# Optimization experiments

Measured on AMD Instinct MI355X. Metric: run time of the kernel, lower is better.

## Reference

```python
import jax, jax.numpy as jnp
import numpy as np
import math

NEG = -1e9


def maximum_path(logp, mask):
    # logp, mask: [B, Tx, Ty]; Viterbi-style monotonic alignment search (VITS MAS)
    B, Tx, Ty = logp.shape
    lp = jnp.where(mask > 0, logp, NEG)
    # forward DP: value[x, y] = lp[x, y] + max(value[x, y-1], value[x-1, y-1])
    v0 = jnp.where(jnp.arange(Tx)[None, :] == 0, lp[:, :, 0], NEG)  # [B, Tx]

    def fwd(v, lp_y):
        v_diag = jnp.pad(v[:, :-1], ((0, 0), (1, 0)), constant_values=NEG)
        take_diag = v_diag > v  # strict >, matches cython 'value[x,y-1] < value[x-1,y-1]'
        return lp_y + jnp.maximum(v, v_diag), take_diag

    lp_rest = jnp.moveaxis(lp[:, :, 1:], 2, 0)  # [Ty-1, B, Tx]
    _, dirs = jax.lax.scan(fwd, v0, lp_rest)
    dirs = jnp.concatenate([jnp.zeros((1, B, Tx), bool), dirs], axis=0)  # [Ty, B, Tx]

    t_x = mask[:, :, 0].sum(axis=1).astype(jnp.int32)  # valid text length per batch
    t_y = mask[:, 0, :].sum(axis=1).astype(jnp.int32)  # valid spec length per batch

    def back(idx, inp):
        dir_y, y = inp  # dir_y [B, Tx], y scalar
        active = (y < t_y)  # [B]
        row = jax.nn.one_hot(idx, Tx, dtype=logp.dtype) * active[:, None].astype(logp.dtype)
        d = jnp.take_along_axis(dir_y, idx[:, None], axis=1)[:, 0]
        idx = jnp.where(active, idx - d.astype(jnp.int32), idx)
        return idx, row

    ys = jnp.arange(Ty - 1, -1, -1)
    _, rows = jax.lax.scan(back, t_x - 1, (dirs[::-1], ys))
    path = jnp.moveaxis(rows[::-1], 0, 2)  # [B, Tx, Ty]
    return path


def _make_masks(x_lengths, y_lengths, Tx, Ty):
    x_len = jnp.clip(x_lengths, 2, Tx)
    y_len = jnp.clip(y_lengths, 2, Ty)
    y_len = jnp.maximum(y_len, x_len)  # MAS needs T_y >= T_x per sample
    x_mask = (jnp.arange(Tx)[None, :] < x_len[:, None]).astype(jnp.float32)  # [B, Tx]
    y_mask = (jnp.arange(Ty)[None, :] < y_len[:, None]).astype(jnp.float32)  # [B, Ty]
    return x_mask, y_mask


def setup_inputs() -> dict:
    key = jax.random.key(0)
    B, C, Tx, Ty = 32, 192, 512, 2048
    k1, k2, k3, k4, k5 = jax.random.split(key, 5)
    z_p = jax.random.normal(k1, (B, C, Ty), dtype=jnp.float32)
    m_p = jax.random.normal(k2, (B, C, Tx), dtype=jnp.float32)
    logs_p = jax.random.normal(k3, (B, C, Tx), dtype=jnp.float32) * 0.3
    x_lengths = jax.random.randint(k4, (B,), Tx // 2, Tx + 1, dtype=jnp.int32)
    y_lengths = jax.random.randint(k5, (B,), Ty // 2, Ty + 1, dtype=jnp.int32)
    return {"z_p": z_p, "m_p": m_p, "logs_p": logs_p, "x_lengths": x_lengths, "y_lengths": y_lengths}


def reference(z_p, m_p, logs_p, x_lengths, y_lengths):
    B, C, Ty = z_p.shape
    Tx = m_p.shape[2]
    x_mask, y_mask = _make_masks(x_lengths, y_lengths, Tx, Ty)
    attn_mask = x_mask[:, :, None] * y_mask[:, None, :]  # [B, Tx, Ty]

    # log N(z_p ; m_p, exp(logs_p)) scored for every (text, spec) pair
    o_scale = jnp.exp(-2.0 * logs_p)  # [B, C, Tx]
    logp1 = jnp.sum(-0.5 * math.log(2.0 * math.pi) - logs_p, axis=1)[:, :, None]  # [B, Tx, 1]
    logp2 = jnp.einsum('bct,bcs->bts', o_scale, -0.5 * z_p ** 2)  # [B, Tx, Ty]
    logp3 = jnp.einsum('bct,bcs->bts', m_p * o_scale, z_p)
    logp4 = jnp.sum(-0.5 * m_p ** 2 * o_scale, axis=1)[:, :, None]
    logp = logp2 + logp3 + logp1 + logp4

    attn = maximum_path(logp, attn_mask)  # [B, Tx, Ty], hard 0/1 alignment
    attn_durations = attn.sum(axis=2)[:, None, :]  # [B, 1, Tx]

    # expand text stats to spec frames: torch.einsum('klmn,kjm->kjn', attn[:,None], m_p)
    m_p_dur = jnp.einsum('bts,bct->bcs', attn, m_p)      # [B, C, Ty]
    logs_p_dur = jnp.einsum('bts,bct->bcs', attn, logs_p)
    return attn_durations, attn[:, None], m_p_dur, logs_p_dur
```

## Files before the change

kernel.cpp:

```cpp
#include <hip/hip_runtime.h>

#define NEGV -1e9f
#define BB 32
#define CC 192
#define TXD 512
#define TYD 2048

#define E_DUR   0
#define E_ATTN  16384
#define E_MP    33570816
#define E_LS    46153728
#define E_TOTAL 58736640

#define OFF_DIRS  6291456

#define WS_PATH 0ull
#define WS_YST  131072ull
#define WS_TXTY 196864ull
#define WS_NEED 262144ull

typedef _Float16 f16x8 __attribute__((ext_vector_type(8)));
typedef float f32x4 __attribute__((ext_vector_type(4)));

__device__ __forceinline__ void glds16(const void* g, void* l) {
    __builtin_amdgcn_global_load_lds((const __attribute__((address_space(1))) unsigned*)g,
                                     (__attribute__((address_space(3))) unsigned*)l, 16, 0, 0);
}
__device__ __forceinline__ unsigned packh(_Float16 a, _Float16 b) {
    union { _Float16 h[2]; unsigned u; } x; x.h[0] = a; x.h[1] = b; return x.u;
}

__global__ __launch_bounds__(256) void k_prepB(const float* __restrict__ logs_p,
                                               const float* __restrict__ m_p,
                                               const int* __restrict__ xl,
                                               const int* __restrict__ yl,
                                               _Float16* __restrict__ Bpl,
                                               float* __restrict__ l14,
                                               unsigned* __restrict__ txty) {
    __shared__ float lst[CC][33];
    __shared__ float mst[CC][33];
    __shared__ float p14[8][32];
    int b = blockIdx.y, t0 = blockIdx.x * 32, tid = threadIdx.x;
    const float* lsb = logs_p + (size_t)b * CC * TXD + t0;
    const float* mb  = m_p    + (size_t)b * CC * TXD + t0;
#pragma unroll
    for (int i = 0; i < 24; ++i) {
        int u = i * 256 + tid, c = u >> 5, t = u & 31;
        lst[c][t] = lsb[(size_t)c * TXD + t];
        mst[c][t] = mb [(size_t)c * TXD + t];
    }
    __syncthreads();
    { int q = tid >> 5, t = tid & 31; float s = 0.f;
      for (int c = q * 24; c < q * 24 + 24; ++c) {
          float ls = lst[c][t], m = mst[c][t];
          float o = expf(-2.f * ls);
          s += -0.918938533204672741780329736406f - ls - 0.5f * m * m * o;
      }
      p14[q][t] = s; }
    __syncthreads();
    if (tid < 32) {
        float s = 0.f;
#pragma unroll
        for (int q = 0; q < 8; ++q) s += p14[q][tid];
        l14[b * TXD + t0 + tid] = s;
    }
    _Float16* Bb = Bpl + (size_t)b * (4 * TXD * CC);
    unsigned* B0 = (unsigned*)(Bb);
    unsigned* B1 = (unsigned*)(Bb + (size_t)1 * TXD * CC);
    unsigned* B2 = (unsigned*)(Bb + (size_t)2 * TXD * CC);
    unsigned* B3 = (unsigned*)(Bb + (size_t)3 * TXD * CC);
#pragma unroll
    for (int i = 0; i < 12; ++i) {
        int u = i * 256 + tid, t = u / 96, cp = u - t * 96, c = cp * 2;
        float ls0 = lst[c][t], ls1 = lst[c + 1][t];
        float m0 = mst[c][t], m1 = mst[c + 1][t];
        float o0 = expf(-2.f * ls0), o1 = expf(-2.f * ls1);
        float w0 = m0 * o0, w1 = m1 * o1;
        _Float16 oh0 = (_Float16)o0, oh1 = (_Float16)o1;
        _Float16 ol0 = (_Float16)(o0 - (float)oh0), ol1 = (_Float16)(o1 - (float)oh1);
        _Float16 wh0 = (_Float16)w0, wh1 = (_Float16)w1;
        _Float16 wl0 = (_Float16)(w0 - (float)wh0), wl1 = (_Float16)(w1 - (float)wh1);
        int ui = ((t0 + t) * CC + c) >> 1;
        B0[ui] = packh(oh0, oh1);
        B1[ui] = packh(ol0, ol1);
        B2[ui] = packh(wh0, wh1);
        B3[ui] = packh(wl0, wl1);
    }
    if (blockIdx.x == 0 && blockIdx.y == 0 && tid < BB) {
        int txv = min(max(xl[tid], 2), TXD);
        int tyv = min(max(yl[tid], 2), TYD);
        tyv = max(tyv, txv);
        txty[tid] = (unsigned)txv;
        txty[BB + tid] = (unsigned)tyv;
    }
}

__global__ __launch_bounds__(256) void k_prepZ(const float* __restrict__ z_p,
                                               _Float16* __restrict__ Zpl, int sBase) {
    __shared__ float zt[CC][65];
    int b = blockIdx.y, s0 = blockIdx.x * 64, tid = threadIdx.x;
    const float* zb = z_p + (size_t)b * CC * TYD + sBase + s0;
#pragma unroll
    for (int i = 0; i < 48; ++i) {
        int u = i * 256 + tid, c = u >> 6, s = u & 63;
        zt[c][s] = zb[(size_t)c * TYD + s];
    }
    __syncthreads();
    _Float16* Zb = Zpl + (size_t)b * (4 * 1024 * CC);
    unsigned* Z0 = (unsigned*)(Zb);
    unsigned* Z1 = (unsigned*)(Zb + (size_t)1 * 1024 * CC);
    unsigned* Z2 = (unsigned*)(Zb + (size_t)2 * 1024 * CC);
    unsigned* Z3 = (unsigned*)(Zb + (size_t)3 * 1024 * CC);
#pragma unroll
    for (int i = 0; i < 24; ++i) {
        int u = i * 256 + tid, s = u / 96, cp = u - s * 96, c = cp * 2;
        float z0 = zt[c][s], z1 = zt[c + 1][s];
        float P0 = -0.5f * z0 * z0, P1 = -0.5f * z1 * z1;
        _Float16 ph0 = (_Float16)P0, ph1 = (_Float16)P1;
        _Float16 pl0 = (_Float16)(P0 - (float)ph0), pl1 = (_Float16)(P1 - (float)ph1);
        _Float16 zh0 = (_Float16)z0, zh1 = (_Float16)z1;
        _Float16 zl0 = (_Float16)(z0 - (float)zh0), zl1 = (_Float16)(z1 - (float)zh1);
        int ui = ((s0 + s) * CC + c) >> 1;
        Z0[ui] = packh(ph0, ph1);
        Z1[ui] = packh(pl0, pl1);
        Z2[ui] = packh(zh0, zh1);
        Z3[ui] = packh(zl0, zl1);
    }
}

__global__ __launch_bounds__(256, 2) void k_mm(const _Float16* __restrict__ Zpl,
                                               const _Float16* __restrict__ Bpl,
                                               const float* __restrict__ l14,
                                               const unsigned* __restrict__ txty,
                                               float* __restrict__ L, int sBase) {
    __shared__ __align__(16) char As[32768];
    __shared__ __align__(16) char Bs[16384];
    int bid = blockIdx.x;
    int xcd = bid & 7, idx = bid >> 3;
    int b = xcd + 8 * (idx >> 4);
    int tile = idx & 15;
    int s0 = (tile >> 2) * 256, t0 = (tile & 3) * 128;
    int txb = (int)txty[b], tyb = (int)txty[BB + b];
    int sg0 = sBase + s0;
    if (sg0 >= tyb) return;
    int tid = threadIdx.x, l = tid & 63, w = tid >> 6;
    float* Lt = L + ((size_t)b * TYD + sg0) * TXD + t0;
    if (t0 >= txb) {
#pragma unroll
        for (int i = 0; i < 32; ++i) {
            int u = i * 256 + tid, r = u >> 5, c4 = (u & 31) * 4;
            *(float4*)(Lt + (size_t)r * TXD + c4) = make_float4(NEGV, NEGV, NEGV, NEGV);
        }
        return;
    }
    f32x4 acc[4][8];
#pragma unroll
    for (int i = 0; i < 4; ++i)
#pragma unroll
        for (int j = 0; j < 8; ++j) acc[i][j] = (f32x4){0.f, 0.f, 0.f, 0.f};

    const char* Zb = (const char*)(Zpl + (size_t)b * (4 * 1024 * CC));
    const char* Bb = (const char*)(Bpl + (size_t)b * (4 * TXD * CC));
    int lrow = l >> 3;
    int gOff = lrow * 384 + (((l & 7) ^ lrow) * 16);
    int arow_off = (w * 64 + (l & 15)) * 128;
    int brow_off = (l & 15) * 128;
    int slot0 = (((l >> 4) + 0) ^ (l & 7)) * 16;
    int slot1 = (((l >> 4) + 4) ^ (l & 7)) * 16;

    for (int pass = 0; pass < 6; ++pass) {
        int ap = ((pass >= 3) ? 2 : 0) + ((pass == 2 || pass == 5) ? 1 : 0);
        int bp = ((pass >= 3) ? 2 : 0) + ((pass == 1 || pass == 4) ? 1 : 0);
        const char* Zp = Zb + ((size_t)ap * 1024 + s0) * 384;
        const char* Bp = Bb + ((size_t)bp * TXD + t0) * 384;
        for (int k0 = 0; k0 < 384; k0 += 128) {
            __syncthreads();
#pragma unroll
            for (int j = 0; j < 8; ++j) {
                int c = w * 8 + j;
                glds16(Zp + (size_t)c * (8 * 384) + gOff + k0, As + c * 1024);
            }
#pragma unroll
            for (int j = 0; j < 4; ++j) {
                int c = w * 4 + j;
                glds16(Bp + (size_t)c * (8 * 384) + gOff + k0, Bs + c * 1024);
            }
            __syncthreads();
#pragma unroll
            for (int ks = 0; ks < 2; ++ks) {
                int so = ks ? slot1 : slot0;
                f16x8 av[4], bv[8];
#pragma unroll
                for (int fm = 0; fm < 4; ++fm)
                    av[fm] = *(const f16x8*)(As + arow_off + fm * (16 * 128) + so);
#pragma unroll
                for (int fn = 0; fn < 8; ++fn)
                    bv[fn] = *(const f16x8*)(Bs + brow_off + fn * (16 * 128) + so);
#pragma unroll
                for (int fm = 0; fm < 4; ++fm)
#pragma unroll
                    for (int fn = 0; fn < 8; ++fn)
                        acc[fm][fn] = __builtin_amdgcn_mfma_f32_16x16x32_f16(
                            av[fm], bv[fn], acc[fm][fn], 0, 0, 0);
            }
        }
    }
    float l14v[8];
#pragma unroll
    for (int fn = 0; fn < 8; ++fn) l14v[fn] = l14[b * TXD + t0 + fn * 16 + (l & 15)];
    int sb = sg0 + w * 64 + (l >> 4) * 4;
    int tcol = t0 + (l & 15);
#pragma unroll
    for (int fm = 0; fm < 4; ++fm)
#pragma unroll
        for (int r = 0; r < 4; ++r) {
            int sg = sb + fm * 16 + r;
            bool sv = sg < tyb;
            float* Lrow = L + ((size_t)b * TYD + sg) * TXD;
#pragma unroll
            for (int fn = 0; fn < 8; ++fn) {
                int t = tcol + fn * 16;
                Lrow[t] = (sv && t < txb) ? (acc[fm][fn][r] + l14v[fn]) : NEGV;
            }
        }
}

__global__ __launch_bounds__(64) void k_dp(const float* __restrict__ L,
                                           const unsigned* __restrict__ txty,
                                           unsigned* __restrict__ dirsG,
                                           unsigned short* __restrict__ pathG,
                                           unsigned* __restrict__ ystartG,
                                           float* __restrict__ outDur) {
    __shared__ unsigned char dmaps[32 * 512];
    __shared__ unsigned short path[TYD];
    __shared__ unsigned cnt[513];
    __shared__ unsigned ebuf[32];
    int b = blockIdx.x, lane = threadIdx.x;
    int tx = (int)txty[b], ty = (int)txty[BB + b];
    const float* Lb = L + (size_t)b * (TYD * TXD);
    unsigned* dGw = dirsG + (size_t)b * (512 * 64);

    float4 aLo[8], aHi[8], bLo[8], bHi[8];
    float v[8];
    unsigned p[8];
    int G8 = (ty + 7) >> 3;

#define LOAD_GRP(LO, HI, GN) do {                                           \
        _Pragma("unroll")                                                   \
        for (int q_ = 0; q_ < 8; ++q_) {                                    \
            int r_ = 8 * (GN) + q_;                                         \
            r_ = (r_ < ty) ? r_ : (ty - 1);                                 \
            const float* rp_ = Lb + (size_t)r_ * TXD + lane * 8;            \
            LO[q_] = *(const float4*)(rp_);                                 \
            HI[q_] = *(const float4*)(rp_ + 4);                             \
        } } while (0)

#define DP_GRP(LO, HI, G_) do {                                             \
        unsigned w0_ = 0, w1_ = 0;                                          \
        _Pragma("unroll")                                                   \
        for (int q_ = 0; q_ < 8; ++q_) {                                    \
            int y_ = 8 * (G_) + q_;                                         \
            if ((G_) == 0 && q_ == 0) {                                     \
                float lp_[8] = {LO[0].x, LO[0].y, LO[0].z, LO[0].w,         \
                                HI[0].x, HI[0].y, HI[0].z, HI[0].w};        \
                _Pragma("unroll")                                           \
                for (int i = 0; i < 8; ++i) {                               \
                    int x_ = lane * 8 + i;                                  \
                    v[i] = (x_ == 0) ? lp_[i] : NEGV;                       \
                    p[i] = (unsigned)x_;                                    \
                }                                                           \
            } else if (y_ < ty) {                                           \
                float cur_[8] = {LO[q_].x, LO[q_].y, LO[q_].z, LO[q_].w,    \
                                 HI[q_].x, HI[q_].y, HI[q_].z, HI[q_].w};   \
                float vp0_ = __int_as_float(__builtin_amdgcn_mov_dpp(       \
                    __float_as_int(v[7]), 0x138, 0xf, 0xf, true));          \
                unsigned pp0_ = (unsigned)__builtin_amdgcn_mov_dpp(         \
                    (int)p[7], 0x138, 0xf, 0xf, true);                      \
                if (lane == 0) vp0_ = NEGV;                                 \
                unsigned bits_ = 0;                                         \
                _Pragma("unroll")                                           \
                for (int i = 7; i >= 0; --i) {                              \
                    float vp_ = (i == 0) ? vp0_ : v[i - 1];                 \
                    unsigned pp_ = (i == 0) ? pp0_ : p[i - 1];              \
                    bool d_ = vp_ > v[i];                                   \
                    v[i] = cur_[i] + (d_ ? vp_ : v[i]);                     \
                    p[i] = d_ ? pp_ : p[i];                                 \
                    bits_ |= (d_ ? 1u : 0u) << i;                           \
                }                                                           \
                if (q_ < 4) w0_ |= bits_ << (8 * q_);                       \
                else        w1_ |= bits_ << (8 * (q_ - 4));                 \
                if (q_ == 0 && ((G_) & 7) == 0 && (G_) != 0) {              \
                    _Pragma("unroll")                                       \
                    for (int i = 0; i < 8; ++i) p[i] = (unsigned)(lane * 8 + i); \
                }                                                           \
                if (q_ == 7 && ((G_) & 7) == 7) {                           \
                    int c_ = y_ >> 6;                                       \
                    _Pragma("unroll")                                       \
                    for (int i = 0; i < 8; ++i)                             \
                        dmaps[c_ * 512 + lane * 8 + i] =                    \
                            (unsigned char)((unsigned)(lane * 8 + i) - p[i]); \
                }                                                           \
            }                                                               \
        }                                                                   \
        dGw[(2 * (G_)) * 64 + lane] = w0_;                                  \
        dGw[(2 * (G_) + 1) * 64 + lane] = w1_;                              \
        } while (0)

    LOAD_GRP(aLo, aHi, 0);
    LOAD_GRP(bLo, bHi, 1);
    for (int g = 0; g < G8; g += 2) {
        DP_GRP(aLo, aHi, g);
        LOAD_GRP(aLo, aHi, g + 2);
        if (g + 1 < G8) {
            DP_GRP(bLo, bHi, g + 1);
            LOAD_GRP(bLo, bHi, g + 3);
        }
    }
#undef LOAD_GRP
#undef DP_GRP
    __syncthreads();

    int c0 = (ty - 1) >> 6;
    if (lane == 0) {
        int pos = tx - 1;
        for (int y = ty - 1; y >= (c0 << 6); --y) {
            path[y] = (unsigned short)pos;
            unsigned wv = dGw[(y >> 2) * 64 + (pos >> 3)];
            pos -= (int)((wv >> (((y & 3) << 3) | (pos & 7))) & 1u);
        }
        for (int c = c0 - 1; c >= 0; --c) {
            ebuf[c] = (unsigned)pos;
            int P = pos - (int)dmaps[c * 512 + pos];
            unsigned wv = dGw[(c << 4) * 64 + (P >> 3)];
            pos = P - (int)((wv >> (P & 7)) & 1u);
        }
    }
    __syncthreads();
    if (lane < c0) {
        int c = lane;
        int pos = (int)ebuf[c];
        for (int y = (c << 6) + 63; y >= (c << 6); --y) {
            path[y] = (unsigned short)pos;
            unsigned wv = dGw[(y >> 2) * 64 + (pos >> 3)];
            pos -= (int)((wv >> (((y & 3) << 3) | (pos & 7))) & 1u);
        }
    }
    __syncthreads();

    for (int i = lane; i < 513; i += 64) cnt[i] = 0;
    __syncthreads();
    for (int y = lane; y < ty; y += 64) atomicAdd(&cnt[path[y]], 1u);
    __syncthreads();

    unsigned c8[8], lsum = 0;
#pragma unroll
    for (int i = 0; i < 8; ++i) {
        c8[i] = cnt[lane * 8 + i];
        lsum += c8[i];
    }
    unsigned incl = lsum;
    for (int d = 1; d < 64; d <<= 1) {
        unsigned t = (unsigned)__shfl_up((int)incl, d);
        if (lane >= d) incl += t;
    }
    unsigned run = incl - lsum;
#pragma unroll
    for (int i = 0; i < 8; ++i) {
        int x = lane * 8 + i;
        ystartG[b * 513 + x] = run;
        outDur[(size_t)b * TXD + x] = (float)c8[i];
        run += c8[i];
    }
    if (lane == 0) ystartG[b * 513 + 512] = (unsigned)ty;
    for (int y = lane; y < ty; y += 64) pathG[b * TYD + y] = path[y];
}

__global__ __launch_bounds__(64) void k_attn(const unsigned* __restrict__ ystartG,
                                             float* __restrict__ out) {
    int x = blockIdx.x, b = blockIdx.y, lane = threadIdx.x;
    unsigned s0 = ystartG[b * 513 + x];
    unsigned s1 = ystartG[b * 513 + x + 1];
    float* row = out + E_ATTN + ((size_t)(b * TXD + x)) * TYD + lane * 32;
#pragma unroll
    for (int k = 0; k < 8; ++k) {
        unsigned y0 = (unsigned)(lane * 32 + k * 4);
        float4 o;
        o.x = (y0 + 0 >= s0 && y0 + 0 < s1) ? 1.0f : 0.0f;
        o.y = (y0 + 1 >= s0 && y0 + 1 < s1) ? 1.0f : 0.0f;
        o.z = (y0 + 2 >= s0 && y0 + 2 < s1) ? 1.0f : 0.0f;
        o.w = (y0 + 3 >= s0 && y0 + 3 < s1) ? 1.0f : 0.0f;
        *(float4*)(row + k * 4) = o;
    }
}

__global__ __launch_bounds__(256) void k_gather(const float* __restrict__ m_p,
                                                const float* __restrict__ logs_p,
                                                const unsigned short* __restrict__ pathG,
                                                const unsigned* __restrict__ txty,
                                                float* __restrict__ out) {
    __shared__ unsigned short px[64];
    int yc = blockIdx.x, b = blockIdx.y;
    int y0 = yc * 64, tid = threadIdx.x;
    int lane = tid & 63, w = tid >> 6;
    int ty = (int)txty[BB + b];
    if (tid < 64) px[tid] = (y0 + tid < ty) ? pathG[b * TYD + y0 + tid] : 0;
    __syncthreads();
    bool act = (y0 + lane) < ty;
    int xx = (int)px[lane];
    for (int c = w; c < CC; c += 4) {
        float mv = act ? m_p[((size_t)b * CC + c) * TXD + xx] : 0.0f;
        float lv = act ? logs_p[((size_t)b * CC + c) * TXD + xx] : 0.0f;
        size_t oidx = ((size_t)(b * CC + c)) * TYD + y0 + lane;
        out[E_MP + oidx] = mv;
        out[E_LS + oidx] = lv;
    }
}

extern "C" void kernel_launch(void* const* d_in, const int* in_sizes, int n_in,
                              void* d_out, int out_size, void* d_ws, size_t ws_size,
                              hipStream_t stream) {
    if (out_size < E_TOTAL) return;
    if (ws_size < WS_NEED) return;
    const float* z_p    = (const float*)d_in[0];
    const float* m_p    = (const float*)d_in[1];
    const float* logs_p = (const float*)d_in[2];
    const int* xl       = (const int*)d_in[3];
    const int* yl       = (const int*)d_in[4];
    float* out = (float*)d_out;
    char* ws = (char*)d_ws;

    float* l14            = out + E_DUR;
    float* L              = out + E_ATTN;
    _Float16* Zpl         = (_Float16*)(out + E_MP);
    _Float16* Bpl         = (_Float16*)(out + E_LS);
    unsigned* dirsG       = (unsigned*)(out + E_LS + OFF_DIRS);
    unsigned short* pathG = (unsigned short*)(ws + WS_PATH);
    unsigned* ystartG     = (unsigned*)(ws + WS_YST);
    unsigned* txty        = (unsigned*)(ws + WS_TXTY);

    hipLaunchKernelGGL(k_prepB, dim3(16, BB), dim3(256), 0, stream,
                       logs_p, m_p, xl, yl, Bpl, l14, txty);
    hipLaunchKernelGGL(k_prepZ, dim3(16, BB), dim3(256), 0, stream, z_p, Zpl, 0);
    hipLaunchKernelGGL(k_mm, dim3(512), dim3(256), 0, stream, Zpl, Bpl, l14, txty, L, 0);
    hipLaunchKernelGGL(k_prepZ, dim3(16, BB), dim3(256), 0, stream, z_p, Zpl, 1024);
    hipLaunchKernelGGL(k_mm, dim3(512), dim3(256), 0, stream, Zpl, Bpl, l14, txty, L, 1024);
    hipLaunchKernelGGL(k_dp, dim3(BB), dim3(64), 0, stream, L, txty, dirsG, pathG, ystartG, out + E_DUR);
    hipLaunchKernelGGL(k_attn, dim3(TXD, BB), dim3(64), 0, stream, ystartG, out);
    hipLaunchKernelGGL(k_gather, dim3(TYD / 64, BB), dim3(256), 0, stream, m_p, logs_p, pathG, txty, out);
}
```

Measured before the change: 545.5 us.

## Add prefetch helper wavefront to DP kernel to warm cache ahead of scan

The DP kernel grows from one to two wavefronts. The second wave walks the L matrix one phase (16 groups of 8 rows) ahead of the compute wave, touching one float per 64-byte line to pull rows into cache. The two waves stay in step through a per-phase __syncthreads. The DP inner step also computes the max with fmaxf instead of a select. This aims to hide global-memory latency on the latency-bound serial scan, at the cost of barrier overhead and extra memory traffic.

Result: slower. 581.9 us (+6.7%).

```diff
diff --git a/kernel.cpp b/kernel.cpp
--- a/kernel.cpp
+++ b/kernel.cpp
@@ -225,25 +225,28 @@
         }
 }
 
-__global__ __launch_bounds__(64) void k_dp(const float* __restrict__ L,
-                                           const unsigned* __restrict__ txty,
-                                           unsigned* __restrict__ dirsG,
-                                           unsigned short* __restrict__ pathG,
-                                           unsigned* __restrict__ ystartG,
-                                           float* __restrict__ outDur) {
+__global__ __launch_bounds__(128) void k_dp(const float* __restrict__ L,
+                                            const unsigned* __restrict__ txty,
+                                            unsigned* __restrict__ dirsG,
+                                            unsigned short* __restrict__ pathG,
+                                            unsigned* __restrict__ ystartG,
+                                            float* __restrict__ outDur) {
     __shared__ unsigned char dmaps[32 * 512];
     __shared__ unsigned short path[TYD];
     __shared__ unsigned cnt[513];
     __shared__ unsigned ebuf[32];
-    int b = blockIdx.x, lane = threadIdx.x;
+    int b = blockIdx.x, tid = threadIdx.x;
+    int lane = tid & 63, wid = tid >> 6;
     int tx = (int)txty[b], ty = (int)txty[BB + b];
     const float* Lb = L + (size_t)b * (TYD * TXD);
     unsigned* dGw = dirsG + (size_t)b * (512 * 64);
-
-    float4 aLo[8], aHi[8], bLo[8], bHi[8];
-    float v[8];
-    unsigned p[8];
     int G8 = (ty + 7) >> 3;
+    int nPhase = (G8 + 15) >> 4;
+
+    if (wid == 0) {
+        float4 aLo[8], aHi[8], bLo[8], bHi[8];
+        float v[8];
+        unsigned p[8];
 
 #define LOAD_GRP(LO, HI, GN) do {                                           \
         _Pragma("unroll")                                                   \
@@ -282,8 +285,9 @@
                 for (int i = 7; i >= 0; --i) {                              \
                     float vp_ = (i == 0) ? vp0_ : v[i - 1];                 \
                     unsigned pp_ = (i == 0) ? pp0_ : p[i - 1];              \
-                    bool d_ = vp_ > v[i];                                   \
-                    v[i] = cur_[i] + (d_ ? vp_ : v[i]);                     \
+                    float vm_ = fmaxf(vp_, v[i]);     \
+                    bool d_ = vp_ > v[i];             \
+                    v[i] = cur_[i] + vm_;                                   \
                     p[i] = d_ ? pp_ : p[i];                                 \
                     bits_ |= (d_ ? 1u : 0u) << i;                           \
                 }                                                           \
@@ -306,22 +310,45 @@
         dGw[(2 * (G_) + 1) * 64 + lane] = w1_;                              \
         } while (0)
 
-    LOAD_GRP(aLo, aHi, 0);
-    LOAD_GRP(bLo, bHi, 1);
-    for (int g = 0; g < G8; g += 2) {
-        DP_GRP(aLo, aHi, g);
-        LOAD_GRP(aLo, aHi, g + 2);
-        if (g + 1 < G8) {
-            DP_GRP(bLo, bHi, g + 1);
-            LOAD_GRP(bLo, bHi, g + 3);
-        }
-    }
+        LOAD_GRP(aLo, aHi, 0);
+        LOAD_GRP(bLo, bHi, 1);
+        int g = 0;
+        for (int ph = 0; ph < nPhase; ++ph) {
+            __syncthreads();
+            int gEnd = (ph + 1) << 4; if (gEnd > G8) gEnd = G8;
+            for (; g < gEnd; g += 2) {
+                DP_GRP(aLo, aHi, g);
+                LOAD_GRP(aLo, aHi, g + 2);
+                if (g + 1 < G8) {
+                    DP_GRP(bLo, bHi, g + 1);
+                    LOAD_GRP(bLo, bHi, g + 3);
+                }
+            }
+        }
 #undef LOAD_GRP
 #undef DP_GRP
+    } else {
+        const char* Lc = (const char*)Lb;
+        float acc = 0.f;
+        for (int gp = 0; gp < 16 && gp < G8; ++gp) {
+            const float* fp = (const float*)(Lc + (size_t)gp * 16384 + (lane << 6));
+            acc += fp[0] + fp[1024] + fp[2048] + fp[3072];
+        }
+        for (int ph = 0; ph < nPhase; ++ph) {
+            __syncthreads();
+            int a = (ph + 1) << 4, bnd = (ph + 2) << 4;
+            if (bnd > G8) bnd = G8;
+            for (int gp = a; gp < bnd; ++gp) {
+                const float* fp = (const float*)(Lc + (size_t)gp * 16384 + (lane << 6));
+                acc += fp[0] + fp[1024] + fp[2048] + fp[3072];
+            }
+        }
+        asm volatile("" :: "v"(acc));
+    }
     __syncthreads();
 
     int c0 = (ty - 1) >> 6;
-    if (lane == 0) {
+    if (tid == 0) {
         int pos = tx - 1;
         for (int y = ty - 1; y >= (c0 << 6); --y) {
             path[y] = (unsigned short)pos;
@@ -336,8 +363,8 @@
         }
     }
     __syncthreads();
-    if (lane < c0) {
-        int c = lane;
+    if (tid < c0) {
+        int c = tid;
         int pos = (int)ebuf[c];
         for (int y = (c << 6) + 63; y >= (c << 6); --y) {
             path[y] = (unsigned short)pos;
@@ -347,32 +374,34 @@
     }
     __syncthreads();
 
-    for (int i = lane; i < 513; i += 64) cnt[i] = 0;
-    __syncthreads();
-    for (int y = lane; y < ty; y += 64) atomicAdd(&cnt[path[y]], 1u);
-    __syncthreads();
-
-    unsigned c8[8], lsum = 0;
-#pragma unroll
-    for (int i = 0; i < 8; ++i) {
-        c8[i] = cnt[lane * 8 + i];
-        lsum += c8[i];
-    }
-    unsigned incl = lsum;
-    for (int d = 1; d < 64; d <<= 1) {
-        unsigned t = (unsigned)__shfl_up((int)incl, d);
-        if (lane >= d) incl += t;
-    }
-    unsigned run = incl - lsum;
-#pragma unroll
-    for (int i = 0; i < 8; ++i) {
-        int x = lane * 8 + i;
-        ystartG[b * 513 + x] = run;
-        outDur[(size_t)b * TXD + x] = (float)c8[i];
-        run += c8[i];
-    }
-    if (lane == 0) ystartG[b * 513 + 512] = (unsigned)ty;
-    for (int y = lane; y < ty; y += 64) pathG[b * TYD + y] = path[y];
+    for (int i = tid; i < 513; i += 128) cnt[i] = 0;
+    __syncthreads();
+    for (int y = tid; y < ty; y += 128) atomicAdd(&cnt[path[y]], 1u);
+    __syncthreads();
+
+    if (wid == 0) {
+        unsigned c8[8], lsum = 0;
+#pragma unroll
+        for (int i = 0; i < 8; ++i) {
+            c8[i] = cnt[lane * 8 + i];
+            lsum += c8[i];
+        }
+        unsigned incl = lsum;
+        for (int d = 1; d < 64; d <<= 1) {
+            unsigned t = (unsigned)__shfl_up((int)incl, d);
+            if (lane >= d) incl += t;
+        }
+        unsigned run = incl - lsum;
+#pragma unroll
+        for (int i = 0; i < 8; ++i) {
+            int x = lane * 8 + i;
+            ystartG[b * 513 + x] = run;
+            outDur[(size_t)b * TXD + x] = (float)c8[i];
+            run += c8[i];
+        }
+        if (lane == 0) ystartG[b * 513 + 512] = (unsigned)ty;
+    }
+    for (int y = tid; y < ty; y += 128) pathG[b * TYD + y] = path[y];
 }
 
 __global__ __launch_bounds__(64) void k_attn(const unsigned* __restrict__ ystartG,
@@ -444,7 +473,7 @@
     hipLaunchKernelGGL(k_mm, dim3(512), dim3(256), 0, stream, Zpl, Bpl, l14, txty, L, 0);
     hipLaunchKernelGGL(k_prepZ, dim3(16, BB), dim3(256), 0, stream, z_p, Zpl, 1024);
     hipLaunchKernelGGL(k_mm, dim3(512), dim3(256), 0, stream, Zpl, Bpl, l14, txty, L, 1024);
-    hipLaunchKernelGGL(k_dp, dim3(BB), dim3(64), 0, stream, L, txty, dirsG, pathG, ystartG, out + E_DUR);
+    hipLaunchKernelGGL(k_dp, dim3(BB), dim3(128), 0, stream, L, txty, dirsG, pathG, ystartG, out + E_DUR);
     hipLaunchKernelGGL(k_attn, dim3(TXD, BB), dim3(64), 0, stream, ystartG, out);
     hipLaunchKernelGGL(k_gather, dim3(TYD / 64, BB), dim3(256), 0, stream, m_p, logs_p, pathG, txty, out);
 }
```
